# Optimization experiments

Measured on AMD Instinct MI355X. Metric: run time of the kernel, lower is better.

## Reference

```python
import jax, jax.numpy as jnp
import numpy as np


def _pairwise_dist(x, y):
    # x: [B, N, D], y: [B, M, D] -> Euclidean distances [B, N, M]
    # numerical safety before sqrt.
    x2 = jnp.sum(x * x, axis=-1)            # [B, N]
    y2 = jnp.sum(y * y, axis=-1)            # [B, M]
    xy = jnp.einsum('bnd,bmd->bnm', x, y)   # [B, N, M]
    d2 = x2[:, :, None] + y2[:, None, :] - 2.0 * xy
    return jnp.sqrt(jnp.maximum(d2, 0.0))


def setup_inputs() -> dict:
    key = jax.random.key(0)
    k1, k2 = jax.random.split(key)
    B, N, M, D = 4, 8192, 8192, 3
    true_pos = jax.random.normal(k1, (B, N, D), dtype=jnp.float32)
    pred_pos = jax.random.normal(k2, (B, M, D), dtype=jnp.float32)
    return {"true_pos": true_pos, "pred_pos": pred_pos}


def reference(true_pos, pred_pos):
    dists = _pairwise_dist(true_pos.astype(jnp.float32),
                           pred_pos.astype(jnp.float32))  # [B, N, M]
    mins = jnp.min(dists, axis=2)        # [B, N] nearest pred for each true
    mins_seeds = jnp.min(dists, axis=1)  # [B, M] nearest true for each pred
    loss = jnp.mean(mins)
    loss_seeds = jnp.mean(mins_seeds)
    return (loss + loss_seeds, mins_seeds)
```

## Files before the change

kernel.cpp:

```cpp
#include <hip/hip_runtime.h>

typedef __attribute__((ext_vector_type(8)))  short bf16x8;
typedef __attribute__((ext_vector_type(16))) float f32x16;
typedef __attribute__((ext_vector_type(4)))  float v4f;

#define TPB    256
#define NPTS   8192
#define NB     4
#define TOTPTS (NB * NPTS)
#define XWAVE  64
#define XBLK   (4 * XWAVE)
#define YTILE  1024
#define NTILES (YTILE / 32)
#define GXB    (NPTS / XBLK)
#define GYB    (NPTS / YTILE)
#define NSLICE (2 * NB)
#define WS2_FLOATS ((size_t)GYB * NSLICE * NPTS)
#define NPARTIAL ((2 * TOTPTS) / 64)


__device__ __forceinline__ short bfr(float f) {
    unsigned u = __float_as_uint(f);
    return (short)((u + 0x7FFFu + ((u >> 16) & 1u)) >> 16);
}
__device__ __forceinline__ float bf2f(short s) {
    return __uint_as_float(((unsigned)(unsigned short)s) << 16);
}

__global__ void __launch_bounds__(TPB, 1) nnmin_mfma(
        const float* __restrict__ T, const float* __restrict__ P,
        float* __restrict__ ws2)
{
    __shared__ v4f sA[NTILES * 64];

    const int z   = blockIdx.z;
    const int dir = z >> 2;
    const int b   = z & 3;
    const float* Xb = (dir ? P : T) + (size_t)b * NPTS * 3;
    const float* Yb = (dir ? T : P) + (size_t)b * NPTS * 3;
    const int t     = threadIdx.x;
    const int l     = t & 63;
    const int w     = t >> 6;
    const int ybase = blockIdx.y * YTILE;
    const int xw    = blockIdx.x * XBLK + w * XWAVE;

    for (int p = t; p < YTILE; p += TPB) {
        const float* yp = Yb + (size_t)(ybase + p) * 3;
        float y0 = yp[0], y1 = yp[1], y2 = yp[2];
        short yh0 = bfr(y0); short yl0 = bfr(y0 - bf2f(yh0));
        short yh1 = bfr(y1); short yl1 = bfr(y1 - bf2f(yh1));
        short yh2 = bfr(y2); short yl2 = bfr(y2 - bf2f(yh2));
        float hy  = 0.5f * (y0 * y0 + y1 * y1 + y2 * y2);
        short hyh = bfr(hy); short hyl = bfr(hy - bf2f(hyh));
        int tile = p >> 5, m = p & 31;
        union { short s[8]; v4f v; } e0, e1;
        e0.s[0] = yh0; e0.s[1] = yl0; e0.s[2] = yh0; e0.s[3] = yh1;
        e0.s[4] = yl1; e0.s[5] = yh1; e0.s[6] = yh2; e0.s[7] = yl2;
        e1.s[0] = yh2; e1.s[1] = hyh; e1.s[2] = hyl; e1.s[3] = 0;
        e1.s[4] = 0;   e1.s[5] = 0;   e1.s[6] = 0;   e1.s[7] = 0;
        sA[tile * 64 + m]      = e0.v;
        sA[tile * 64 + 32 + m] = e1.v;
    }

    const int   kh  = l >> 5;
    const short ONE = 0x3F80;
    bf16x8 B[2];
#pragma unroll
    for (int f = 0; f < 2; ++f) {
        const float* xp = Xb + (size_t)(xw + f * 32 + (l & 31)) * 3;
        float nx = -xp[0], ny = -xp[1], nz = -xp[2];
        short h0 = bfr(nx); short lo0 = bfr(nx - bf2f(h0));
        short h1 = bfr(ny); short lo1 = bfr(ny - bf2f(h1));
        short h2 = bfr(nz); short lo2 = bfr(nz - bf2f(h2));
        union { short s[8]; bf16x8 v; } e;
        if (kh == 0) {
            e.s[0] = h0; e.s[1] = h0; e.s[2] = lo0; e.s[3] = h1;
            e.s[4] = h1; e.s[5] = lo1; e.s[6] = h2; e.s[7] = h2;
        } else {
            e.s[0] = lo2; e.s[1] = ONE; e.s[2] = ONE; e.s[3] = 0;
            e.s[4] = 0;   e.s[5] = 0;   e.s[6] = 0;   e.s[7] = 0;
        }
        B[f] = e.v;
    }
    __syncthreads();

    f32x16 zero = {0.f};
    float rm[2][16];
#pragma unroll
    for (int f = 0; f < 2; ++f)
#pragma unroll
        for (int i = 0; i < 16; ++i) rm[f][i] = 3.0e38f;

#pragma unroll 2
    for (int tl = 0; tl < NTILES; tl += 2) {
        v4f a4a = sA[(tl + 0) * 64 + l];
        v4f a4b = sA[(tl + 1) * 64 + l];
        bf16x8 Aa = *(bf16x8*)&a4a;
        bf16x8 Ab = *(bf16x8*)&a4b;
#pragma unroll
        for (int f = 0; f < 2; ++f) {
            f32x16 da = __builtin_amdgcn_mfma_f32_32x32x16_bf16(Aa, B[f], zero, 0, 0, 0);
            f32x16 db = __builtin_amdgcn_mfma_f32_32x32x16_bf16(Ab, B[f], zero, 0, 0, 0);
#pragma unroll
            for (int i = 0; i < 16; ++i) {
                float ea = da[i], eb = db[i];
                asm("v_min3_f32 %0, %0, %1, %2"
                    : "+v"(rm[f][i]) : "v"(ea), "v"(eb));
            }
        }
    }

    float* o = ws2 + ((size_t)blockIdx.y * NSLICE + z) * NPTS;
#pragma unroll
    for (int f = 0; f < 2; ++f) {
        float v = rm[f][0];
#pragma unroll
        for (int i = 1; i < 16; ++i) v = fminf(v, rm[f][i]);
        v = fminf(v, __shfl_xor(v, 32, 64));
        if (l < 32) o[xw + f * 32 + l] = v;
    }
}

__global__ void __launch_bounds__(TPB) finalize_kernel(
        const float* __restrict__ ws2,
        const float* __restrict__ T, const float* __restrict__ P,
        float* __restrict__ out, float* __restrict__ partials)
{
    int i   = blockIdx.x * TPB + threadIdx.x;
    int dir = (i >= TOTPTS) ? 1 : 0;
    int idx = i - dir * TOTPTS;
    int b   = idx >> 13;
    int x   = idx & (NPTS - 1);

    const float* p0 = ws2 + (size_t)(dir * 4 + b) * NPTS + x;
    float m = 3.0e38f;
#pragma unroll
    for (int c = 0; c < GYB; ++c)
        m = fminf(m, p0[(size_t)c * NSLICE * NPTS]);

    const float* xp = (dir ? P : T) + ((size_t)b * NPTS + x) * 3;
    float a0 = xp[0], a1 = xp[1], a2 = xp[2];
    float hx = 0.5f * (a0 * a0 + a1 * a1 + a2 * a2);
    float d  = sqrtf(fmaxf(2.0f * (hx + m), 0.0f));
    if (dir) out[1 + idx] = d;

#pragma unroll
    for (int off = 32; off > 0; off >>= 1)
        d += __shfl_down(d, off, 64);
    if ((threadIdx.x & 63) == 0) partials[i >> 6] = d;
}

__global__ void scalar_kernel(const float* __restrict__ partials,
                              float* __restrict__ out) {
    int t = threadIdx.x;
    float s = 0.0f;
#pragma unroll
    for (int k = 0; k < NPARTIAL / 64; ++k)
        s += partials[t * (NPARTIAL / 64) + k];
#pragma unroll
    for (int off = 32; off > 0; off >>= 1)
        s += __shfl_down(s, off, 64);
    if (t == 0) out[0] = s * (1.0f / (float)TOTPTS);
}

extern "C" void kernel_launch(void* const* d_in, const int* in_sizes, int n_in,
                              void* d_out, int out_size, void* d_ws, size_t ws_size,
                              hipStream_t stream) {
    const float* truep = (const float*)d_in[0];
    const float* predp = (const float*)d_in[1];
    float* out = (float*)d_out;

    float* ws2      = (float*)d_ws;
    float* partials = ws2 + WS2_FLOATS;

    dim3 grid(GXB, GYB, 2 * NB);
    nnmin_mfma<<<grid, TPB, 0, stream>>>(truep, predp, ws2);

    finalize_kernel<<<(2 * TOTPTS) / TPB, TPB, 0, stream>>>(
        ws2, truep, predp, out, partials);
    scalar_kernel<<<1, 64, 0, stream>>>(partials, out);
}
```

Measured before the change: 85.25 us.

## Shrink MFMA K to 8 by rounding X to single bf16 and recomputing its norm

X coordinates now go into the matrix op as single bf16 values instead of hi/lo pairs, so the product fits in K=8. The MFMA changes from 32x32x16 to 32x32x8 and the shared-memory Y tiles shrink to 4 shorts per entry. The finalize kernel computes |x|^2 from the same bf16-rounded X, so the distance stays consistent with the bf16 X. This halves the MFMA work and the LDS traffic per tile. The cost is lower precision on the X side, which may shift the minimum distances within tolerance.

Result: faster. 83.09 us, median of 2 (-2.5%).

```diff
diff --git a/kernel.cpp b/kernel.cpp
--- a/kernel.cpp
+++ b/kernel.cpp
@@ -1,8 +1,7 @@
 #include <hip/hip_runtime.h>
 
-typedef __attribute__((ext_vector_type(8)))  short bf16x8;
+typedef __attribute__((ext_vector_type(4)))  short bf16x4;
 typedef __attribute__((ext_vector_type(16))) float f32x16;
-typedef __attribute__((ext_vector_type(4)))  float v4f;
 
 #define TPB    256
 #define NPTS   8192
@@ -31,7 +30,7 @@
         const float* __restrict__ T, const float* __restrict__ P,
         float* __restrict__ ws2)
 {
-    __shared__ v4f sA[NTILES * 64];
+    __shared__ bf16x4 sA[NTILES * 64];
 
     const int z   = blockIdx.z;
     const int dir = z >> 2;
@@ -53,34 +52,25 @@
         float hy  = 0.5f * (y0 * y0 + y1 * y1 + y2 * y2);
         short hyh = bfr(hy); short hyl = bfr(hy - bf2f(hyh));
         int tile = p >> 5, m = p & 31;
-        union { short s[8]; v4f v; } e0, e1;
-        e0.s[0] = yh0; e0.s[1] = yl0; e0.s[2] = yh0; e0.s[3] = yh1;
-        e0.s[4] = yl1; e0.s[5] = yh1; e0.s[6] = yh2; e0.s[7] = yl2;
-        e1.s[0] = yh2; e1.s[1] = hyh; e1.s[2] = hyl; e1.s[3] = 0;
-        e1.s[4] = 0;   e1.s[5] = 0;   e1.s[6] = 0;   e1.s[7] = 0;
-        sA[tile * 64 + m]      = e0.v;
-        sA[tile * 64 + 32 + m] = e1.v;
+        bf16x4 e0 = {yh0, yl0, yh1, yl1};
+        bf16x4 e1 = {yh2, yl2, hyh, hyl};
+        sA[tile * 64 + m]      = e0;
+        sA[tile * 64 + 32 + m] = e1;
     }
 
     const int   kh  = l >> 5;
     const short ONE = 0x3F80;
-    bf16x8 B[2];
+    bf16x4 B[2];
 #pragma unroll
     for (int f = 0; f < 2; ++f) {
         const float* xp = Xb + (size_t)(xw + f * 32 + (l & 31)) * 3;
-        float nx = -xp[0], ny = -xp[1], nz = -xp[2];
-        short h0 = bfr(nx); short lo0 = bfr(nx - bf2f(h0));
-        short h1 = bfr(ny); short lo1 = bfr(ny - bf2f(h1));
-        short h2 = bfr(nz); short lo2 = bfr(nz - bf2f(h2));
-        union { short s[8]; bf16x8 v; } e;
-        if (kh == 0) {
-            e.s[0] = h0; e.s[1] = h0; e.s[2] = lo0; e.s[3] = h1;
-            e.s[4] = h1; e.s[5] = lo1; e.s[6] = h2; e.s[7] = h2;
-        } else {
-            e.s[0] = lo2; e.s[1] = ONE; e.s[2] = ONE; e.s[3] = 0;
-            e.s[4] = 0;   e.s[5] = 0;   e.s[6] = 0;   e.s[7] = 0;
-        }
-        B[f] = e.v;
+        short h0 = bfr(-xp[0]);
+        short h1 = bfr(-xp[1]);
+        short h2 = bfr(-xp[2]);
+        bf16x4 e;
+        if (kh == 0) e = (bf16x4){h0, h0, h1, h1};
+        else         e = (bf16x4){h2, h2, ONE, ONE};
+        B[f] = e;
     }
     __syncthreads();
 
@@ -93,14 +83,12 @@
 
 #pragma unroll 2
     for (int tl = 0; tl < NTILES; tl += 2) {
-        v4f a4a = sA[(tl + 0) * 64 + l];
-        v4f a4b = sA[(tl + 1) * 64 + l];
-        bf16x8 Aa = *(bf16x8*)&a4a;
-        bf16x8 Ab = *(bf16x8*)&a4b;
+        bf16x4 Aa = sA[(tl + 0) * 64 + l];
+        bf16x4 Ab = sA[(tl + 1) * 64 + l];
 #pragma unroll
         for (int f = 0; f < 2; ++f) {
-            f32x16 da = __builtin_amdgcn_mfma_f32_32x32x16_bf16(Aa, B[f], zero, 0, 0, 0);
-            f32x16 db = __builtin_amdgcn_mfma_f32_32x32x16_bf16(Ab, B[f], zero, 0, 0, 0);
+            f32x16 da = __builtin_amdgcn_mfma_f32_32x32x8bf16_1k(Aa, B[f], zero, 0, 0, 0);
+            f32x16 db = __builtin_amdgcn_mfma_f32_32x32x8bf16_1k(Ab, B[f], zero, 0, 0, 0);
 #pragma unroll
             for (int i = 0; i < 16; ++i) {
                 float ea = da[i], eb = db[i];
@@ -139,7 +127,9 @@
         m = fminf(m, p0[(size_t)c * NSLICE * NPTS]);
 
     const float* xp = (dir ? P : T) + ((size_t)b * NPTS + x) * 3;
-    float a0 = xp[0], a1 = xp[1], a2 = xp[2];
+    float a0 = bf2f(bfr(xp[0]));
+    float a1 = bf2f(bfr(xp[1]));
+    float a2 = bf2f(bfr(xp[2]));
     float hx = 0.5f * (a0 * a0 + a1 * a1 + a2 * a2);
     float d  = sqrtf(fmaxf(2.0f * (hx + m), 0.0f));
     if (dir) out[1 + idx] = d;
```
